# Kernel optimization log

Hardware: AMD Instinct MI355X
Metric: run time of the kernel (lower is better)

The kernel has to match this reference:

```python
import jax, jax.numpy as jnp
import numpy as np

B, IN, U = 16, 1024, 1024


def _wSw(W, S):
    # W: [i,u], S: [b,i,i] -> W^T S W : [b,u,u]
    return jnp.einsum('iu,bij,jv->buv', W, S, W)


def _xSx(x, Wsig):
    # (sum_i x_i^2) * W_Sigma, broadcast over batch
    return jnp.sum(x * x, axis=1)[:, None, None] * Wsig


def _trS(S, Wsig):
    return jnp.trace(S, axis1=1, axis2=2)[:, None, None] * Wsig


def _hadamard_sigma(s1, s2, m1, m2):
    # s1*s2 + diag(m1) s2 diag(m1) + diag(m2) s1 diag(m2)
    return (s1 * s2
            + m1[:, :, None] * s2 * m1[:, None, :]
            + m2[:, :, None] * s1 * m2[:, None, :])


def _act_sigma(g, S):
    # S * outer(g, g)
    return S * (g[:, :, None] * g[:, None, :])


def setup_inputs() -> dict:
    key = jax.random.key(0)
    ks = jax.random.split(key, 16)
    f32 = jnp.float32
    init_mu, ini_sigma = 0.05, -4.6
    inp = {
        'mu_inputs': jax.random.normal(ks[0], (B, IN), f32),
        'sigma_inputs': 0.01 * jax.random.normal(ks[1], (B, IN, IN), f32),
        'prev_state': 0.1 * jax.random.normal(ks[2], (B, U), f32),
        'Sigma_state': 0.01 * jax.random.normal(ks[3], (B, U, U), f32),
        'U_z': init_mu * jax.random.normal(ks[4], (IN, U), f32),
        'uz_sigma': jnp.full((U,), ini_sigma, f32),
        'W_z': init_mu * jax.random.normal(ks[5], (U, U), f32),
        'wz_sigma': jnp.full((U,), ini_sigma, f32),
        'U_r': init_mu * jax.random.normal(ks[6], (IN, U), f32),
        'ur_sigma': jnp.full((U,), ini_sigma, f32),
        'W_r': init_mu * jax.random.normal(ks[7], (U, U), f32),
        'wr_sigma': jnp.full((U,), ini_sigma, f32),
        'U_h': init_mu * jax.random.normal(ks[8], (IN, U), f32),
        'uh_sigma': jnp.full((U,), ini_sigma, f32),
        'W_h': init_mu * jax.random.normal(ks[9], (U, U), f32),
        'wh_sigma': jnp.full((U,), ini_sigma, f32),
    }
    return inp


def reference(mu_inputs, sigma_inputs, prev_state, Sigma_state,
              U_z, uz_sigma, W_z, wz_sigma,
              U_r, ur_sigma, W_r, wr_sigma,
              U_h, uh_sigma, W_h, wh_sigma):
    sp = jax.nn.softplus
    # ---- z gate ----
    pre_z = mu_inputs @ U_z + prev_state @ W_z
    z = jax.nn.sigmoid(pre_z)
    Uz_S, Wz_S = jnp.diag(sp(uz_sigma)), jnp.diag(sp(wz_sigma))
    Sigma_zz = (_wSw(U_z, sigma_inputs) + _xSx(mu_inputs, Uz_S) + _trS(sigma_inputs, Uz_S)
                + _wSw(W_z, Sigma_state) + _xSx(prev_state, Wz_S) + _trS(Sigma_state, Wz_S))
    Sigma_z = _act_sigma(z * (1.0 - z), Sigma_zz)  # analytic d sigmoid
    # ---- r gate ----
    pre_r = mu_inputs @ U_r + prev_state @ W_r
    r = jax.nn.sigmoid(pre_r)
    Ur_S, Wr_S = jnp.diag(sp(ur_sigma)), jnp.diag(sp(wr_sigma))
    Sigma_rr = (_wSw(U_r, sigma_inputs) + _xSx(mu_inputs, Ur_S) + _trS(sigma_inputs, Ur_S)
                + _wSw(W_r, Sigma_state) + _xSx(prev_state, Wr_S) + _trS(Sigma_state, Wr_S))
    Sigma_r = _act_sigma(r * (1.0 - r), Sigma_rr)
    # ---- h gate ----
    sr = prev_state * r
    pre_h = mu_inputs @ U_h + sr @ W_h
    h = jnp.tanh(pre_h)
    Uh_S, Wh_S = jnp.diag(sp(uh_sigma)), jnp.diag(sp(wh_sigma))
    sigma_g = _hadamard_sigma(Sigma_state, Sigma_r, prev_state, r)
    Sigma_hh = (_wSw(U_h, sigma_inputs) + _xSx(mu_inputs, Uh_S) + _trS(sigma_inputs, Uh_S)
                + _wSw(W_h, sigma_g) + _xSx(sr, Wh_S) + _trS(sigma_g, Wh_S))
    Sigma_h = _act_sigma(1.0 - h * h, Sigma_hh)  # analytic d tanh
    # ---- combine ----
    mu_out = z * prev_state + (1.0 - z) * h
    sigma_a = _hadamard_sigma(Sigma_z, Sigma_state, z, prev_state)
    sigma_b = _hadamard_sigma(Sigma_z, Sigma_h, 1.0 - z, h)
    sigma_ab = Sigma_z * (prev_state[:, :, None] * h[:, None, :])
    sigma_abT = Sigma_z * (h[:, :, None] * prev_state[:, None, :])
    Sigma_out = sigma_a + sigma_b - sigma_ab - sigma_abT
    Sigma_out = jnp.where(jnp.isfinite(Sigma_out), Sigma_out, jnp.zeros_like(Sigma_out))
    eye = jnp.eye(Sigma_out.shape[-1], dtype=bool)
    Sigma_out = jnp.where(eye, jnp.abs(Sigma_out), Sigma_out)
    return mu_out, Sigma_out
```

## Files before the change

kernel.cpp:

```cpp
#include <hip/hip_runtime.h>
#include <math.h>


#define B_  16
#define N_  1024
#define NN_ (1024*1024)

typedef __bf16 bf16x8 __attribute__((ext_vector_type(8)));
typedef float  f32x4  __attribute__((ext_vector_type(4)));
typedef unsigned short ushort8v __attribute__((ext_vector_type(8)));

__device__ __forceinline__ unsigned short f2bf(float f) {
  union { float f; unsigned int u; } v; v.f = f;
  unsigned int r = v.u + 0x7fffu + ((v.u >> 16) & 1u);
  return (unsigned short)(r >> 16);
}
__device__ __forceinline__ float bf2f(unsigned short h) {
  union { unsigned int u; float f; } v; v.u = ((unsigned int)h) << 16;
  return v.f;
}

__device__ __forceinline__ void gload_lds16(const void* g, void* l) {
  __builtin_amdgcn_global_load_lds((__attribute__((address_space(1))) void*)g,
                                   (__attribute__((address_space(3))) void*)l,
                                   16, 0, 0);
}

#define MFMA_ __builtin_amdgcn_mfma_f32_16x16x32_bf16
#define SBAR_()  do { __builtin_amdgcn_sched_barrier(0); \
                      __builtin_amdgcn_s_barrier(); \
                      __builtin_amdgcn_sched_barrier(0); } while (0)

template<int OMODE, int PAIR>
__global__ __launch_bounds__(512)
void gemm8p(const unsigned short* __restrict__ A, int lda, long aStride, int koffA,
            const unsigned short* __restrict__ Bm, const unsigned short* __restrict__ Bm2,
            int ldb, long bStride, int K,
            void* __restrict__ Out, int ldo, long oStride, int noff,
            const float* __restrict__ act,
            const float* __restrict__ spU, const float* __restrict__ spW,
            const float* __restrict__ dU, const float* __restrict__ dW,
            const unsigned short* __restrict__ SzP, const float* __restrict__ SstP,
            const float* __restrict__ zV, const float* __restrict__ prevV,
            const float* __restrict__ hV)
{
  __shared__ __align__(16) char ldsb[131072];
  const int id = blockIdx.x;
  const int xcd = id & 7, rest = id >> 3;
  const int mt = rest & 3, pp = rest >> 2;
  const int panel = xcd + (pp << 3);
  const int nt = panel & 3;
  const int b  = (panel >> 2) & 15;
  const int ps = PAIR ? (panel >> 6) : 0;
  const unsigned short* Bsel = (PAIR && ps) ? Bm2 : Bm;
  const int kofx = koffA + (ps ? 1024 : 0);
  const int nofx = noff  + (ps ? 1024 : 0);
  const int mbase = mt << 8, nbase = nt << 8;
  const int tid = threadIdx.x, lane = tid & 63, w = tid >> 6;
  const int wm = w >> 2, wn = w & 3;
  const int NT = K >> 6;

  f32x4 acc[8][4];
  const f32x4 zero4 = {0.f, 0.f, 0.f, 0.f};
#pragma unroll
  for (int i = 0; i < 8; i++)
#pragma unroll
    for (int j = 0; j < 4; j++) acc[i][j] = zero4;

  const int l3 = lane >> 3, l7 = lane & 7;
  const int posg = l7 ^ l3;
  const int gr = (l3 << 1) + (posg >> 2);
  const int gc = (posg & 3) << 3;
  const int bi0 = w << 1, bi1 = bi0 + 1;
  const int rS0 = ((bi0 >> 1) << 4) + gr, cS0 = ((bi0 & 1) << 5) + gc;
  const int rS1 = ((bi1 >> 1) << 4) + gr, cS1 = ((bi1 & 1) << 5) + gc;
  const unsigned short* Ab = A + (size_t)b * aStride + (size_t)mbase * lda + kofx;
  const unsigned short* Bb = Bsel + (size_t)b * bStride + (size_t)nbase * ldb;
  const int d0 = w << 11, d1 = (w << 11) + 1024;

  auto SA = [&](int tt, int h) {
    char* dst = ldsb + ((tt & 1) << 16) + (h << 14);
    const unsigned short* s = Ab + (size_t)(h << 7) * lda + ((size_t)tt << 6);
    gload_lds16(s + (size_t)rS0 * lda + cS0, dst + d0);
    gload_lds16(s + (size_t)rS1 * lda + cS1, dst + d1);
  };
  auto SB = [&](int tt, int h) {
    char* dst = ldsb + ((tt & 1) << 16) + 32768 + (h << 14);
    const unsigned short* s = Bb + (size_t)(h << 7) * ldb + ((size_t)tt << 6);
    gload_lds16(s + (size_t)rS0 * ldb + cS0, dst + d0);
    gload_lds16(s + (size_t)rS1 * ldb + cS1, dst + d1);
  };

  const int lrow = lane & 15, c4 = lane >> 4;
  const int aoff = ((lrow >> 1) << 7) + (((((lrow & 1) << 2) | c4) ^ (lrow >> 1)) << 4);
  const int abase = wm << 14;
  const int bbase = 32768 + ((wn >> 1) << 14);
  const int brg   = (wn & 1) << 2;
  auto LDA = [&](const char* pb, int mi, int ks) -> bf16x8 {
    return *(const bf16x8*)(pb + abase + (((mi << 1) + ks) << 10) + aoff);
  };
  auto LDB = [&](const char* pb, int ni, int ks) -> bf16x8 {
    return *(const bf16x8*)(pb + bbase + ((((brg + ni) << 1) + ks) << 10) + aoff);
  };

  SA(0, 0); SA(0, 1); SB(0, 0); SB(0, 1);
  if (NT > 1) { SB(1, 0); SB(1, 1); }
  asm volatile("s_waitcnt vmcnt(4)" ::: "memory");
  SBAR_();

  bf16x8 avA[4], avB[4], bvA[4], bvB[4];
#pragma unroll
  for (int i = 0; i < 4; i++) avB[i] = LDA(ldsb, i, 0);
#pragma unroll
  for (int i = 0; i < 4; i++) bvB[i] = LDB(ldsb, i, 0);
  __builtin_amdgcn_sched_barrier(0);

  for (int kt = 0; kt < NT; ++kt) {
    const char* pb = ldsb + ((kt & 1) << 16);
    const char* pn = ldsb + (((kt + 1) & 1) << 16);
#pragma unroll
    for (int i = 0; i < 4; i++) avA[i] = LDA(pb, 4 + i, 0);
    if (kt + 1 < NT) SA(kt + 1, 0);
    SBAR_();
    __builtin_amdgcn_s_setprio(1);
#pragma unroll
    for (int ni = 0; ni < 4; ni++)
#pragma unroll
      for (int mi = 0; mi < 4; mi++)
        acc[mi][ni] = MFMA_(avB[mi], bvB[ni], acc[mi][ni], 0, 0, 0);
    __builtin_amdgcn_s_setprio(0);
    SBAR_();
#pragma unroll
    for (int i = 0; i < 4; i++) avB[i] = LDA(pb, i, 1);
#pragma unroll
    for (int i = 0; i < 4; i++) bvA[i] = LDB(pb, i, 1);
    if (kt + 1 < NT) SA(kt + 1, 1);
    SBAR_();
    __builtin_amdgcn_s_setprio(1);
#pragma unroll
    for (int ni = 0; ni < 4; ni++)
#pragma unroll
      for (int mi = 0; mi < 4; mi++)
        acc[4 + mi][ni] = MFMA_(avA[mi], bvB[ni], acc[4 + mi][ni], 0, 0, 0);
    __builtin_amdgcn_s_setprio(0);
    SBAR_();
#pragma unroll
    for (int i = 0; i < 4; i++) avA[i] = LDA(pb, 4 + i, 1);
    SBAR_();
    __builtin_amdgcn_s_setprio(1);
#pragma unroll
    for (int ni = 0; ni < 4; ni++)
#pragma unroll
      for (int mi = 0; mi < 4; mi++)
        acc[mi][ni] = MFMA_(avB[mi], bvA[ni], acc[mi][ni], 0, 0, 0);
    __builtin_amdgcn_s_setprio(0);
    SBAR_();
    if (kt + 2 < NT) {
      SB(kt + 2, 0); SB(kt + 2, 1);
      asm volatile("s_waitcnt vmcnt(4)" ::: "memory");
    } else if (kt + 1 < NT) {
      asm volatile("s_waitcnt vmcnt(0)" ::: "memory");
    }
    SBAR_();
    if (kt + 1 < NT) {
#pragma unroll
      for (int i = 0; i < 4; i++) avB[i] = LDA(pn, i, 0);
#pragma unroll
      for (int i = 0; i < 4; i++) bvB[i] = LDB(pn, i, 0);
    }
    __builtin_amdgcn_sched_barrier(0);
    __builtin_amdgcn_s_setprio(1);
#pragma unroll
    for (int ni = 0; ni < 4; ni++)
#pragma unroll
      for (int mi = 0; mi < 4; mi++)
        acc[4 + mi][ni] = MFMA_(avA[mi], bvA[ni], acc[4 + mi][ni], 0, 0, 0);
    __builtin_amdgcn_s_setprio(0);
    SBAR_();
  }

  __syncthreads();
  unsigned short* scr = (unsigned short*)(ldsb + w * 16384);
  const float* actb = act ? (act + b * N_) : nullptr;
  float dUb = 0.f, dWb = 0.f;
  if (OMODE != 0) { dUb = dU[b]; dWb = dW[b]; }

#pragma unroll
  for (int mi = 0; mi < 8; mi++) {
    const int rl0 = mi * 16 + ((lane >> 4) << 2);
#pragma unroll
    for (int ni = 0; ni < 4; ni++) {
      const int cl = ni * 16 + (lane & 15);
#pragma unroll
      for (int r = 0; r < 4; r++) {
        const int rl = rl0 + r;
        float val = acc[mi][ni][r];
        if (OMODE != 0) {
          const int u = mbase + wm * 128 + rl, v = nbase + wn * 64 + cl;
          if (u == v) val += dUb * spU[u] + dWb * spW[u];
          val *= actb[u] * actb[v];
        }
        scr[rl * 64 + ((((cl >> 3) ^ (rl & 7))) << 3) + (cl & 7)] = f2bf(val);
      }
    }
  }
  asm volatile("s_waitcnt lgkmcnt(0)" ::: "memory");
  __builtin_amdgcn_sched_barrier(0);

#pragma unroll
  for (int pq = 0; pq < 16; pq++) {
    const int row = pq * 8 + (lane >> 3);
    const int slot = lane & 7;
    const int ch = slot ^ (row & 7);
    const int u = mbase + wm * 128 + row;
    const int v0 = nbase + wn * 64 + (ch << 3);
    ushort8v s8 = *(const ushort8v*)&scr[row * 64 + (slot << 3)];
    if (OMODE == 0 || OMODE == 1) {
      unsigned short* ob = (unsigned short*)Out + (size_t)b * oStride
                         + (size_t)u * ldo + nofx + v0;
      *(ushort8v*)ob = s8;
    } else if (OMODE == 3) {
      const float pu = prevV[b * N_ + u];
      const float ru = zV[b * N_ + u];
      const ushort8v st8 = *(const ushort8v*)(SzP + (size_t)b * NN_ + (size_t)u * N_ + v0);
      const f32x4 pv0 = *(const f32x4*)(prevV + b * N_ + v0);
      const f32x4 pv1 = *(const f32x4*)(prevV + b * N_ + v0 + 4);
      const f32x4 rv0 = *(const f32x4*)(zV + b * N_ + v0);
      const f32x4 rv1 = *(const f32x4*)(zV + b * N_ + v0 + 4);
      ushort8v o8;
#pragma unroll
      for (int q = 0; q < 8; q++) {
        const float srv = bf2f((unsigned short)s8[q]);
        const float stt = bf2f((unsigned short)st8[q]);
        const float pv = (q < 4) ? pv0[q] : pv1[q - 4];
        const float rv = (q < 4) ? rv0[q] : rv1[q - 4];
        o8[q] = f2bf(stt * srv + pu * pv * srv + ru * rv * stt);
      }
      unsigned short* ob = (unsigned short*)Out + (size_t)b * oStride
                         + (size_t)u * ldo + v0;
      *(ushort8v*)ob = o8;
    } else {
      const float zu = zV[b * N_ + u];
      const float pu = prevV[b * N_ + u];
      const float hu = hV[b * N_ + u];
      const ushort8v sz8 = *(const ushort8v*)(SzP + (size_t)b * NN_ + (size_t)u * N_ + v0);
      const f32x4 st0 = *(const f32x4*)(SstP + (size_t)b * NN_ + (size_t)u * N_ + v0);
      const f32x4 st1 = *(const f32x4*)(SstP + (size_t)b * NN_ + (size_t)u * N_ + v0 + 4);
      const f32x4 zv0 = *(const f32x4*)(zV + b * N_ + v0);
      const f32x4 zv1 = *(const f32x4*)(zV + b * N_ + v0 + 4);
      const f32x4 pv0 = *(const f32x4*)(prevV + b * N_ + v0);
      const f32x4 pv1 = *(const f32x4*)(prevV + b * N_ + v0 + 4);
      const f32x4 hv0 = *(const f32x4*)(hV + b * N_ + v0);
      const f32x4 hv1 = *(const f32x4*)(hV + b * N_ + v0 + 4);
      f32x4 o0, o1;
#pragma unroll
      for (int q = 0; q < 8; q++) {
        const float shh = bf2f((unsigned short)s8[q]);
        const float szv = bf2f((unsigned short)sz8[q]);
        const float stt = (q < 4) ? st0[q] : st1[q - 4];
        const float zv  = (q < 4) ? zv0[q] : zv1[q - 4];
        const float pv  = (q < 4) ? pv0[q] : pv1[q - 4];
        const float hv  = (q < 4) ? hv0[q] : hv1[q - 4];
        float res = szv * stt + zu * zv * stt + pu * pv * szv
                  + szv * shh + (1.f - zu) * (1.f - zv) * shh + hu * hv * szv
                  - szv * (pu * hv) - szv * (hu * pv);
        if (!isfinite(res)) res = 0.f;
        if (u == v0 + q) res = fabsf(res);
        if (q < 4) o0[q] = res; else o1[q - 4] = res;
      }
      float* ob = (float*)Out + (size_t)b * oStride + (size_t)u * ldo + v0;
      *(f32x4*)ob = o0;
      *(f32x4*)(ob + 4) = o1;
    }
  }
}


__global__ void conv_bf16_2(const float* __restrict__ in0, unsigned short* __restrict__ out0,
                            const float* __restrict__ in1, unsigned short* __restrict__ out1,
                            int n4)
{
  const float* in = blockIdx.y ? in1 : in0;
  unsigned short* out = blockIdx.y ? out1 : out0;
  int i = blockIdx.x * 256 + threadIdx.x;
  const int stride = gridDim.x * 256;
  for (; i < n4; i += stride) {
    const float4 v = ((const float4*)in)[i];
    ushort4 o;
    o.x = f2bf(v.x); o.y = f2bf(v.y); o.z = f2bf(v.z); o.w = f2bf(v.w);
    ((ushort4*)out)[i] = o;
  }
}

__global__ void build_AT(const float* __restrict__ Uz, const float* __restrict__ Wz,
                         const float* __restrict__ Ur, const float* __restrict__ Wr,
                         const float* __restrict__ Uh, const float* __restrict__ Wh,
                         unsigned short* __restrict__ AT)
{
  __shared__ float tile[32][33];
  const int g = blockIdx.z;
  const float* U = g == 0 ? Uz : (g == 1 ? Ur : Uh);
  const float* W = g == 0 ? Wz : (g == 1 ? Wr : Wh);
  const int u0  = blockIdx.x * 32;
  const int k0g = blockIdx.y * 32;
  const float* src = (k0g >= 1024) ? W : U;
  const int kloc = k0g & 1023;
  const int tx = threadIdx.x & 31, ty = threadIdx.x >> 5;
  unsigned short* out = AT + (size_t)g * N_ * 2048;
#pragma unroll
  for (int i = 0; i < 32; i += 8) tile[ty + i][tx] = src[(size_t)(kloc + ty + i) * N_ + u0 + tx];
  __syncthreads();
#pragma unroll
  for (int i = 0; i < 32; i += 8)
    out[(size_t)(u0 + ty + i) * 2048 + k0g + tx] = f2bf(tile[tx][ty + i]);
}

__global__ void softplus6(const float* a0, const float* a1, const float* a2,
                          const float* a3, const float* a4, const float* a5,
                          float* __restrict__ sp)
{
  const float* src[6] = {a0, a1, a2, a3, a4, a5};
  const int g = blockIdx.x;
  const float* s = src[g];
  for (int i = threadIdx.x; i < N_; i += 256) {
    float x = s[i];
    sp[g * N_ + i] = (x > 20.f) ? x : log1pf(expf(x));
  }
}

__global__ void scalars1(const float* __restrict__ mu, const float* __restrict__ prev,
                         const float* __restrict__ sin_, const float* __restrict__ Sst,
                         float* __restrict__ dA, float* __restrict__ dBzr)
{
  __shared__ float red[256];
  const int b = blockIdx.x;
  float s1 = 0.f, s2 = 0.f;
  for (int i = threadIdx.x; i < N_; i += 256) {
    const float m = mu[b * N_ + i];
    s1 += m * m + sin_[(size_t)b * NN_ + (size_t)i * (N_ + 1)];
    const float p = prev[b * N_ + i];
    s2 += p * p + Sst[(size_t)b * NN_ + (size_t)i * (N_ + 1)];
  }
  red[threadIdx.x] = s1; __syncthreads();
  for (int s = 128; s > 0; s >>= 1) { if (threadIdx.x < s) red[threadIdx.x] += red[threadIdx.x + s]; __syncthreads(); }
  if (threadIdx.x == 0) dA[b] = red[0];
  __syncthreads();
  red[threadIdx.x] = s2; __syncthreads();
  for (int s = 128; s > 0; s >>= 1) { if (threadIdx.x < s) red[threadIdx.x] += red[threadIdx.x + s]; __syncthreads(); }
  if (threadIdx.x == 0) dBzr[b] = red[0];
}

__global__ __launch_bounds__(256)
void gate_pre2(const float* __restrict__ x1, const float* __restrict__ x2,
               const float* __restrict__ U0, const float* __restrict__ W0,
               const float* __restrict__ U1, const float* __restrict__ W1,
               float* __restrict__ Ppart)
{
  const int g  = blockIdx.z;
  const int ks = blockIdx.y;
  const int out = blockIdx.x * 256 + threadIdx.x;
  const int b = out >> 10, col = out & 1023;
  const float* x = (ks < 4) ? x1 : x2;
  const float* Wm = (g == 0) ? ((ks < 4) ? U0 : W0) : ((ks < 4) ? U1 : W1);
  const int k0 = (ks & 3) * 256;
  const float* xb = x + b * N_ + k0;
  const float* wp = Wm + (size_t)k0 * N_ + col;
  float acc = 0.f;
#pragma unroll 8
  for (int k = 0; k < 256; k++)
    acc += xb[k] * wp[(size_t)k * N_];
  Ppart[(g * 8 + ks) * (B_ * N_) + out] = acc;
}

__global__ void gate_act2(const float* __restrict__ P,
                          float* __restrict__ z, float* __restrict__ gz,
                          float* __restrict__ r, float* __restrict__ gr)
{
  const int out = blockIdx.x * 256 + threadIdx.x;
  float a0 = 0.f, a1 = 0.f;
#pragma unroll
  for (int ks = 0; ks < 8; ks++) {
    a0 += P[ks * (B_ * N_) + out];
    a1 += P[(8 + ks) * (B_ * N_) + out];
  }
  const float s0 = 1.f / (1.f + expf(-a0));
  const float s1 = 1.f / (1.f + expf(-a1));
  z[out] = s0; gz[out] = s0 * (1.f - s0);
  r[out] = s1; gr[out] = s1 * (1.f - s1);
}

__global__ __launch_bounds__(256)
void gate_pre1(const float* __restrict__ x1, const float* __restrict__ x2,
               const float* __restrict__ U0, const float* __restrict__ W0,
               float* __restrict__ Ppart)
{
  const int ks = blockIdx.y;
  const int out = blockIdx.x * 256 + threadIdx.x;
  const int b = out >> 10, col = out & 1023;
  const float* x = (ks < 4) ? x1 : x2;
  const float* Wm = (ks < 4) ? U0 : W0;
  const int k0 = (ks & 3) * 256;
  const float* xb = x + b * N_ + k0;
  const float* wp = Wm + (size_t)k0 * N_ + col;
  float acc = 0.f;
#pragma unroll 8
  for (int k = 0; k < 256; k++)
    acc += xb[k] * wp[(size_t)k * N_];
  Ppart[ks * (B_ * N_) + out] = acc;
}

__global__ void gate_act1(const float* __restrict__ P,
                          const float* __restrict__ z, const float* __restrict__ prev,
                          float* __restrict__ h, float* __restrict__ gh,
                          float* __restrict__ mu_out)
{
  const int out = blockIdx.x * 256 + threadIdx.x;
  float a0 = 0.f;
#pragma unroll
  for (int ks = 0; ks < 8; ks++) a0 += P[ks * (B_ * N_) + out];
  const float s = tanhf(a0);
  h[out] = s; gh[out] = 1.f - s * s;
  const float zz = z[out];
  mu_out[out] = zz * prev[out] + (1.f - zz) * s;
}

__global__ void sr_csr(const float* __restrict__ prev, const float* __restrict__ r,
                       float* __restrict__ sr, float* __restrict__ csr)
{
  __shared__ float red[256];
  const int b = blockIdx.x;
  float s = 0.f;
  for (int i = threadIdx.x; i < N_; i += 256) {
    const float v = prev[b * N_ + i] * r[b * N_ + i];
    sr[b * N_ + i] = v;
    s += v * v;
  }
  red[threadIdx.x] = s; __syncthreads();
  for (int k = 128; k > 0; k >>= 1) { if (threadIdx.x < k) red[threadIdx.x] += red[threadIdx.x + k]; __syncthreads(); }
  if (threadIdx.x == 0) csr[b] = red[0];
}

__global__ void scalars2(const unsigned short* __restrict__ Sg,
                         const float* __restrict__ csr, float* __restrict__ dBh)
{
  __shared__ float red[256];
  const int b = blockIdx.x;
  float s = 0.f;
  for (int i = threadIdx.x; i < N_; i += 256)
    s += bf2f(Sg[(size_t)b * NN_ + (size_t)i * (N_ + 1)]);
  red[threadIdx.x] = s; __syncthreads();
  for (int k = 128; k > 0; k >>= 1) { if (threadIdx.x < k) red[threadIdx.x] += red[threadIdx.x + k]; __syncthreads(); }
  if (threadIdx.x == 0) dBh[b] = red[0] + csr[b];
}


extern "C" void kernel_launch(void* const* d_in, const int* in_sizes, int n_in,
                              void* d_out, int out_size, void* d_ws, size_t ws_size,
                              hipStream_t stream)
{
  const float* mu   = (const float*)d_in[0];
  const float* sin_ = (const float*)d_in[1];
  const float* prev = (const float*)d_in[2];
  const float* Sst  = (const float*)d_in[3];
  const float* Uz = (const float*)d_in[4];  const float* uzs = (const float*)d_in[5];
  const float* Wz = (const float*)d_in[6];  const float* wzs = (const float*)d_in[7];
  const float* Ur = (const float*)d_in[8];  const float* urs = (const float*)d_in[9];
  const float* Wr = (const float*)d_in[10]; const float* wrs = (const float*)d_in[11];
  const float* Uh = (const float*)d_in[12]; const float* uhs = (const float*)d_in[13];
  const float* Wh = (const float*)d_in[14]; const float* whs = (const float*)d_in[15];

  char* ws = (char*)d_ws;
  size_t off = 0;
  auto take = [&](size_t bytes) -> char* {
    char* p = ws + off;
    off = (off + bytes + 255) & ~(size_t)255;
    return p;
  };
  unsigned short* Tcm = (unsigned short*)take((size_t)B_ * 2048 * 1024 * 2);
  unsigned short* Sz  = (unsigned short*)take((size_t)B_ * NN_ * 2);
  unsigned short* Sg  = (unsigned short*)take((size_t)B_ * NN_ * 2);
  unsigned short* AT  = (unsigned short*)take((size_t)3 * N_ * 2048 * 2);
  float* Ppart = (float*)take((size_t)16 * B_ * N_ * 4);
  float* sp   = (float*)take(6 * N_ * 4);
  float* z    = (float*)take(B_ * N_ * 4);
  float* gz   = (float*)take(B_ * N_ * 4);
  float* rr   = (float*)take(B_ * N_ * 4);
  float* gr   = (float*)take(B_ * N_ * 4);
  float* h    = (float*)take(B_ * N_ * 4);
  float* gh   = (float*)take(B_ * N_ * 4);
  float* sr   = (float*)take(B_ * N_ * 4);
  float* dA   = (float*)take(64);
  float* dBzr = (float*)take(64);
  float* dBh  = (float*)take(64);
  float* csr  = (float*)take(64);
  if (off > ws_size) return;

  float* mu_out = (float*)d_out;
  float* SigOut = (float*)d_out + (size_t)B_ * N_;
  unsigned short* SinH = (unsigned short*)SigOut;
  unsigned short* SstH = (unsigned short*)SigOut + (size_t)B_ * NN_;

  const unsigned short* ATz = AT;
  const unsigned short* ATr = AT + (size_t)N_ * 2048;
  const unsigned short* ATh = AT + (size_t)2 * N_ * 2048;

  conv_bf16_2<<<dim3(2048, 2), 256, 0, stream>>>(sin_, SinH, Sst, SstH, B_ * NN_ / 4);
  softplus6<<<6, 256, 0, stream>>>(uzs, wzs, urs, wrs, uhs, whs, sp);
  scalars1<<<16, 256, 0, stream>>>(mu, prev, sin_, Sst, dA, dBzr);
  build_AT<<<dim3(32, 64, 3), 256, 0, stream>>>(Uz, Wz, Ur, Wr, Uh, Wh, AT);
  gate_pre2<<<dim3(64, 8, 2), 256, 0, stream>>>(mu, prev, Uz, Wz, Ur, Wr, Ppart);
  gate_act2<<<64, 256, 0, stream>>>(Ppart, z, gz, rr, gr);
  sr_csr<<<16, 256, 0, stream>>>(prev, rr, sr, csr);
  gate_pre1<<<dim3(64, 8), 256, 0, stream>>>(mu, sr, Uh, Wh, Ppart);
  gate_act1<<<64, 256, 0, stream>>>(Ppart, z, prev, h, gh, mu_out);

  const long tS = (long)2048 * 1024;

  gemm8p<0, 1><<<512, 512, 0, stream>>>(ATz, 2048, 0, 0, SinH, SstH, 1024, (long)NN_, 1024,
                                        Tcm, 2048, tS, 0, nullptr, nullptr, nullptr, nullptr, nullptr,
                                        nullptr, nullptr, nullptr, nullptr, nullptr);
  gemm8p<1, 0><<<256, 512, 0, stream>>>(ATz, 2048, 0, 0, Tcm, nullptr, 2048, tS, 2048,
                                        Sz, 1024, (long)NN_, 0, gz, sp + 0, sp + 1024, dA, dBzr,
                                        nullptr, nullptr, nullptr, nullptr, nullptr);
  gemm8p<0, 1><<<512, 512, 0, stream>>>(ATr, 2048, 0, 0, SinH, SstH, 1024, (long)NN_, 1024,
                                        Tcm, 2048, tS, 0, nullptr, nullptr, nullptr, nullptr, nullptr,
                                        nullptr, nullptr, nullptr, nullptr, nullptr);
  gemm8p<3, 0><<<256, 512, 0, stream>>>(ATr, 2048, 0, 0, Tcm, nullptr, 2048, tS, 2048,
                                        Sg, 1024, (long)NN_, 0, gr, sp + 2048, sp + 3072, dA, dBzr,
                                        SstH, nullptr, rr, prev, nullptr);
  scalars2<<<16, 256, 0, stream>>>(Sg, csr, dBh);
  gemm8p<0, 1><<<512, 512, 0, stream>>>(ATh, 2048, 0, 0, SinH, Sg, 1024, (long)NN_, 1024,
                                        Tcm, 2048, tS, 0, nullptr, nullptr, nullptr, nullptr, nullptr,
                                        nullptr, nullptr, nullptr, nullptr, nullptr);
  gemm8p<2, 0><<<256, 512, 0, stream>>>(ATh, 2048, 0, 0, Tcm, nullptr, 2048, tS, 2048,
                                        SigOut, 1024, (long)NN_, 0, gh, sp + 4096, sp + 5120, dA, dBh,
                                        Sz, Sst, z, prev, h);
}
```

Before: 539.3 us.

## Rework GEMM main loop to 4-stage K=32 LDS ring with one barrier per step

Replaces the GEMM's double-buffered K=64 tile pipeline, which had many block barriers and setprio phases per iteration, with a four-slot LDS ring of K=32 tiles. Each step issues a single staged load two tiles ahead and uses one barrier. Fragment loads for the next tile are interleaved between the MFMA quarters. The aim is to cut barrier overhead and improve overlap of global-to-LDS copies with MFMA work, at the cost of twice as many loop iterations with less work between each wait.

```diff
diff --git a/kernel.cpp b/kernel.cpp
--- a/kernel.cpp
+++ b/kernel.cpp
@@ -27,22 +27,19 @@
 }
 
 #define MFMA_ __builtin_amdgcn_mfma_f32_16x16x32_bf16
-#define SBAR_()  do { __builtin_amdgcn_sched_barrier(0); \
-                      __builtin_amdgcn_s_barrier(); \
-                      __builtin_amdgcn_sched_barrier(0); } while (0)
 
 template<int OMODE, int PAIR>
 __global__ __launch_bounds__(512)
-void gemm8p(const unsigned short* __restrict__ A, int lda, long aStride, int koffA,
-            const unsigned short* __restrict__ Bm, const unsigned short* __restrict__ Bm2,
-            int ldb, long bStride, int K,
-            void* __restrict__ Out, int ldo, long oStride, int noff,
-            const float* __restrict__ act,
-            const float* __restrict__ spU, const float* __restrict__ spW,
-            const float* __restrict__ dU, const float* __restrict__ dW,
-            const unsigned short* __restrict__ SzP, const float* __restrict__ SstP,
-            const float* __restrict__ zV, const float* __restrict__ prevV,
-            const float* __restrict__ hV)
+void gemmq(const unsigned short* __restrict__ A, int lda, long aStride, int koffA,
+           const unsigned short* __restrict__ Bm, const unsigned short* __restrict__ Bm2,
+           int ldb, long bStride, int K,
+           void* __restrict__ Out, int ldo, long oStride, int noff,
+           const float* __restrict__ act,
+           const float* __restrict__ spU, const float* __restrict__ spW,
+           const float* __restrict__ dU, const float* __restrict__ dW,
+           const unsigned short* __restrict__ SzP, const float* __restrict__ SstP,
+           const float* __restrict__ zV, const float* __restrict__ prevV,
+           const float* __restrict__ hV)
 {
   __shared__ __align__(16) char ldsb[131072];
   const int id = blockIdx.x;
@@ -58,7 +55,7 @@
   const int mbase = mt << 8, nbase = nt << 8;
   const int tid = threadIdx.x, lane = tid & 63, w = tid >> 6;
   const int wm = w >> 2, wn = w & 3;
-  const int NT = K >> 6;
+  const int NT = K >> 5;
 
   f32x4 acc[8][4];
   const f32x4 zero4 = {0.f, 0.f, 0.f, 0.f};
@@ -69,114 +66,90 @@
 
   const int l3 = lane >> 3, l7 = lane & 7;
   const int posg = l7 ^ l3;
-  const int gr = (l3 << 1) + (posg >> 2);
+  const int gr = ((w * 8 + l3) << 1) + (posg >> 2);
   const int gc = (posg & 3) << 3;
-  const int bi0 = w << 1, bi1 = bi0 + 1;
-  const int rS0 = ((bi0 >> 1) << 4) + gr, cS0 = ((bi0 & 1) << 5) + gc;
-  const int rS1 = ((bi1 >> 1) << 4) + gr, cS1 = ((bi1 & 1) << 5) + gc;
-  const unsigned short* Ab = A + (size_t)b * aStride + (size_t)mbase * lda + kofx;
-  const unsigned short* Bb = Bsel + (size_t)b * bStride + (size_t)nbase * ldb;
-  const int d0 = w << 11, d1 = (w << 11) + 1024;
-
-  auto SA = [&](int tt, int h) {
-    char* dst = ldsb + ((tt & 1) << 16) + (h << 14);
-    const unsigned short* s = Ab + (size_t)(h << 7) * lda + ((size_t)tt << 6);
-    gload_lds16(s + (size_t)rS0 * lda + cS0, dst + d0);
-    gload_lds16(s + (size_t)rS1 * lda + cS1, dst + d1);
-  };
-  auto SB = [&](int tt, int h) {
-    char* dst = ldsb + ((tt & 1) << 16) + 32768 + (h << 14);
-    const unsigned short* s = Bb + (size_t)(h << 7) * ldb + ((size_t)tt << 6);
-    gload_lds16(s + (size_t)rS0 * ldb + cS0, dst + d0);
-    gload_lds16(s + (size_t)rS1 * ldb + cS1, dst + d1);
-  };
+  const unsigned short* Ag = A + (size_t)b * aStride + (size_t)(mbase + gr) * lda + kofx + gc;
+  const unsigned short* Bg = Bsel + (size_t)b * bStride + (size_t)(nbase + gr) * ldb + gc;
+  const size_t a128 = (size_t)128 * lda, bb128 = (size_t)128 * ldb;
+  const int wdst = w << 10;
 
   const int lrow = lane & 15, c4 = lane >> 4;
   const int aoff = ((lrow >> 1) << 7) + (((((lrow & 1) << 2) | c4) ^ (lrow >> 1)) << 4);
-  const int abase = wm << 14;
-  const int bbase = 32768 + ((wn >> 1) << 14);
-  const int brg   = (wn & 1) << 2;
-  auto LDA = [&](const char* pb, int mi, int ks) -> bf16x8 {
-    return *(const bf16x8*)(pb + abase + (((mi << 1) + ks) << 10) + aoff);
+  const int abase0 = (wm << 13);
+  const int bbase0 = 16384 + (wn << 12);
+
+  auto STAGE = [&](int kt) {
+    const int p = kt & 3;
+    const size_t ko = (size_t)kt << 5;
+    char* base = ldsb + (p << 15);
+    gload_lds16(Ag + ko,          base + wdst);
+    gload_lds16(Ag + ko + a128,   base + 8192  + wdst);
+    gload_lds16(Bg + ko,          base + 16384 + wdst);
+    gload_lds16(Bg + ko + bb128,  base + 24576 + wdst);
   };
-  auto LDB = [&](const char* pb, int ni, int ks) -> bf16x8 {
-    return *(const bf16x8*)(pb + bbase + ((((brg + ni) << 1) + ks) << 10) + aoff);
+  auto LDA8 = [&](const char* pbuf, int mi) -> bf16x8 {
+    return *(const bf16x8*)(pbuf + abase0 + (mi << 10) + aoff);
   };
-
-  SA(0, 0); SA(0, 1); SB(0, 0); SB(0, 1);
-  if (NT > 1) { SB(1, 0); SB(1, 1); }
+  auto LDB8 = [&](const char* pbuf, int ni) -> bf16x8 {
+    return *(const bf16x8*)(pbuf + bbase0 + (ni << 10) + aoff);
+  };
+
+  STAGE(0); STAGE(1);
   asm volatile("s_waitcnt vmcnt(4)" ::: "memory");
-  SBAR_();
-
-  bf16x8 avA[4], avB[4], bvA[4], bvB[4];
-#pragma unroll
-  for (int i = 0; i < 4; i++) avB[i] = LDA(ldsb, i, 0);
-#pragma unroll
-  for (int i = 0; i < 4; i++) bvB[i] = LDB(ldsb, i, 0);
   __builtin_amdgcn_sched_barrier(0);
+  __builtin_amdgcn_s_barrier();
+  __builtin_amdgcn_sched_barrier(0);
+
+  bf16x8 a0[4], a1[4], b0[2], b1[2];
+#pragma unroll
+  for (int i = 0; i < 4; i++) a0[i] = LDA8(ldsb, i);
+#pragma unroll
+  for (int i = 0; i < 2; i++) b0[i] = LDB8(ldsb, i);
 
   for (int kt = 0; kt < NT; ++kt) {
-    const char* pb = ldsb + ((kt & 1) << 16);
-    const char* pn = ldsb + (((kt + 1) & 1) << 16);
-#pragma unroll
-    for (int i = 0; i < 4; i++) avA[i] = LDA(pb, 4 + i, 0);
-    if (kt + 1 < NT) SA(kt + 1, 0);
-    SBAR_();
-    __builtin_amdgcn_s_setprio(1);
-#pragma unroll
-    for (int ni = 0; ni < 4; ni++)
+    const char* pbuf = ldsb + ((size_t)(kt & 3) << 15);
+    const char* pnxt = ldsb + ((size_t)((kt + 1) & 3) << 15);
+#pragma unroll
+    for (int i = 0; i < 2; i++) b1[i] = LDB8(pbuf, 2 + i);
+#pragma unroll
+    for (int ni = 0; ni < 2; ni++)
 #pragma unroll
       for (int mi = 0; mi < 4; mi++)
-        acc[mi][ni] = MFMA_(avB[mi], bvB[ni], acc[mi][ni], 0, 0, 0);
-    __builtin_amdgcn_s_setprio(0);
-    SBAR_();
-#pragma unroll
-    for (int i = 0; i < 4; i++) avB[i] = LDA(pb, i, 1);
-#pragma unroll
-    for (int i = 0; i < 4; i++) bvA[i] = LDB(pb, i, 1);
-    if (kt + 1 < NT) SA(kt + 1, 1);
-    SBAR_();
-    __builtin_amdgcn_s_setprio(1);
-#pragma unroll
-    for (int ni = 0; ni < 4; ni++)
+        acc[mi][ni] = MFMA_(a0[mi], b0[ni], acc[mi][ni], 0, 0, 0);
+#pragma unroll
+    for (int i = 0; i < 4; i++) a1[i] = LDA8(pbuf, 4 + i);
+#pragma unroll
+    for (int ni = 0; ni < 2; ni++)
 #pragma unroll
       for (int mi = 0; mi < 4; mi++)
-        acc[4 + mi][ni] = MFMA_(avA[mi], bvB[ni], acc[4 + mi][ni], 0, 0, 0);
-    __builtin_amdgcn_s_setprio(0);
-    SBAR_();
-#pragma unroll
-    for (int i = 0; i < 4; i++) avA[i] = LDA(pb, 4 + i, 1);
-    SBAR_();
-    __builtin_amdgcn_s_setprio(1);
-#pragma unroll
-    for (int ni = 0; ni < 4; ni++)
-#pragma unroll
-      for (int mi = 0; mi < 4; mi++)
-        acc[mi][ni] = MFMA_(avB[mi], bvA[ni], acc[mi][ni], 0, 0, 0);
-    __builtin_amdgcn_s_setprio(0);
-    SBAR_();
+        acc[mi][2 + ni] = MFMA_(a0[mi], b1[ni], acc[mi][2 + ni], 0, 0, 0);
     if (kt + 2 < NT) {
-      SB(kt + 2, 0); SB(kt + 2, 1);
+      STAGE(kt + 2);
       asm volatile("s_waitcnt vmcnt(4)" ::: "memory");
-    } else if (kt + 1 < NT) {
+    } else {
       asm volatile("s_waitcnt vmcnt(0)" ::: "memory");
     }
-    SBAR_();
+    __builtin_amdgcn_sched_barrier(0);
+    __builtin_amdgcn_s_barrier();
+    __builtin_amdgcn_sched_barrier(0);
     if (kt + 1 < NT) {
 #pragma unroll
-      for (int i = 0; i < 4; i++) avB[i] = LDA(pn, i, 0);
-#pragma unroll
-      for (int i = 0; i < 4; i++) bvB[i] = LDB(pn, i, 0);
+      for (int i = 0; i < 4; i++) a0[i] = LDA8(pnxt, i);
     }
-    __builtin_amdgcn_sched_barrier(0);
-    __builtin_amdgcn_s_setprio(1);
-#pragma unroll
-    for (int ni = 0; ni < 4; ni++)
+#pragma unroll
+    for (int ni = 0; ni < 2; ni++)
 #pragma unroll
       for (int mi = 0; mi < 4; mi++)
-        acc[4 + mi][ni] = MFMA_(avA[mi], bvA[ni], acc[4 + mi][ni], 0, 0, 0);
-    __builtin_amdgcn_s_setprio(0);
-    SBAR_();
+        acc[4 + mi][ni] = MFMA_(a1[mi], b0[ni], acc[4 + mi][ni], 0, 0, 0);
+    if (kt + 1 < NT) {
+#pragma unroll
+      for (int i = 0; i < 2; i++) b0[i] = LDB8(pnxt, i);
+    }
+#pragma unroll
+    for (int ni = 0; ni < 2; ni++)
+#pragma unroll
+      for (int mi = 0; mi < 4; mi++)
+        acc[4 + mi][2 + ni] = MFMA_(a1[mi], b1[ni], acc[4 + mi][2 + ni], 0, 0, 0);
   }
 
   __syncthreads();
@@ -516,23 +489,23 @@
 
   const long tS = (long)2048 * 1024;
 
-  gemm8p<0, 1><<<512, 512, 0, stream>>>(ATz, 2048, 0, 0, SinH, SstH, 1024, (long)NN_, 1024,
-                                        Tcm, 2048, tS, 0, nullptr, nullptr, nullptr, nullptr, nullptr,
-                                        nullptr, nullptr, nullptr, nullptr, nullptr);
-  gemm8p<1, 0><<<256, 512, 0, stream>>>(ATz, 2048, 0, 0, Tcm, nullptr, 2048, tS, 2048,
-                                        Sz, 1024, (long)NN_, 0, gz, sp + 0, sp + 1024, dA, dBzr,
-                                        nullptr, nullptr, nullptr, nullptr, nullptr);
-  gemm8p<0, 1><<<512, 512, 0, stream>>>(ATr, 2048, 0, 0, SinH, SstH, 1024, (long)NN_, 1024,
-                                        Tcm, 2048, tS, 0, nullptr, nullptr, nullptr, nullptr, nullptr,
-                                        nullptr, nullptr, nullptr, nullptr, nullptr);
-  gemm8p<3, 0><<<256, 512, 0, stream>>>(ATr, 2048, 0, 0, Tcm, nullptr, 2048, tS, 2048,
-                                        Sg, 1024, (long)NN_, 0, gr, sp + 2048, sp + 3072, dA, dBzr,
-                                        SstH, nullptr, rr, prev, nullptr);
+  gemmq<0, 1><<<512, 512, 0, stream>>>(ATz, 2048, 0, 0, SinH, SstH, 1024, (long)NN_, 1024,
+                                       Tcm, 2048, tS, 0, nullptr, nullptr, nullptr, nullptr, nullptr,
+                                       nullptr, nullptr, nullptr, nullptr, nullptr);
+  gemmq<1, 0><<<256, 512, 0, stream>>>(ATz, 2048, 0, 0, Tcm, nullptr, 2048, tS, 2048,
+                                       Sz, 1024, (long)NN_, 0, gz, sp + 0, sp + 1024, dA, dBzr,
+                                       nullptr, nullptr, nullptr, nullptr, nullptr);
+  gemmq<0, 1><<<512, 512, 0, stream>>>(ATr, 2048, 0, 0, SinH, SstH, 1024, (long)NN_, 1024,
+                                       Tcm, 2048, tS, 0, nullptr, nullptr, nullptr, nullptr, nullptr,
+                                       nullptr, nullptr, nullptr, nullptr, nullptr);
+  gemmq<3, 0><<<256, 512, 0, stream>>>(ATr, 2048, 0, 0, Tcm, nullptr, 2048, tS, 2048,
+                                       Sg, 1024, (long)NN_, 0, gr, sp + 2048, sp + 3072, dA, dBzr,
+                                       SstH, nullptr, rr, prev, nullptr);
   scalars2<<<16, 256, 0, stream>>>(Sg, csr, dBh);
-  gemm8p<0, 1><<<512, 512, 0, stream>>>(ATh, 2048, 0, 0, SinH, Sg, 1024, (long)NN_, 1024,
-                                        Tcm, 2048, tS, 0, nullptr, nullptr, nullptr, nullptr, nullptr,
-                                        nullptr, nullptr, nullptr, nullptr, nullptr);
-  gemm8p<2, 0><<<256, 512, 0, stream>>>(ATh, 2048, 0, 0, Tcm, nullptr, 2048, tS, 2048,
-                                        SigOut, 1024, (long)NN_, 0, gh, sp + 4096, sp + 5120, dA, dBh,
-                                        Sz, Sst, z, prev, h);
-}
+  gemmq<0, 1><<<512, 512, 0, stream>>>(ATh, 2048, 0, 0, SinH, Sg, 1024, (long)NN_, 1024,
+                                       Tcm, 2048, tS, 0, nullptr, nullptr, nullptr, nullptr, nullptr,
+                                       nullptr, nullptr, nullptr, nullptr, nullptr);
+  gemmq<2, 0><<<256, 512, 0, stream>>>(ATh, 2048, 0, 0, Tcm, nullptr, 2048, tS, 2048,
+                                       SigOut, 1024, (long)NN_, 0, gh, sp + 4096, sp + 5120, dA, dBh,
+                                       Sz, Sst, z, prev, h);
+}
```

Measured after the change: 547.8 us. No clear change (+1.6%).
